# Kernel tuning notes

Measured on AMD Instinct MI355X. Metric: run time of the kernel, lower is better.

Reference implementation:

```python
import jax, jax.numpy as jnp
import numpy as np

N_DRUG, N_TARGET, N_EDGES, H = 50000, 20000, 500000, 256


def setup_inputs() -> dict:
    key = jax.random.key(0)
    ks = jax.random.split(key, 6)
    s = 1.0 / np.sqrt(2 * H)
    return {
        "z_drug": jax.random.normal(ks[0], (N_DRUG, H), dtype=jnp.float32),
        "z_target": jax.random.normal(ks[1], (N_TARGET, H), dtype=jnp.float32),
        "row": jax.random.randint(ks[2], (N_EDGES,), 0, N_DRUG, dtype=jnp.int64),
        "col": jax.random.randint(ks[3], (N_EDGES,), 0, N_TARGET, dtype=jnp.int64),
        "W1": jax.random.normal(ks[4], (2 * H, H), dtype=jnp.float32) * s,
        "b1": jnp.zeros((H,), dtype=jnp.float32),
        "W2": jax.random.normal(ks[5], (H, 1), dtype=jnp.float32) * (1.0 / np.sqrt(H)),
        "b2": jnp.zeros((1,), dtype=jnp.float32),
    }


def reference(z_drug, z_target, row, col, W1, b1, W2, b2):
    # gather endpoint embeddings by edge index, concat -> [E, 2H]
    zc = jnp.concatenate([z_drug[row], z_target[col]], axis=-1)
    h = jax.nn.relu(zc @ W1 + b1)          # [E, H]
    return h @ W2 + b2                     # [E, 1]
```

## Files before the change

### kernel.cpp

```cpp
#include <hip/hip_runtime.h>
#include <hip/hip_bf16.h>
#include <stdint.h>


typedef unsigned short u16;
typedef __attribute__((ext_vector_type(8))) short short8;
typedef __attribute__((ext_vector_type(4))) float f32x4;

#define HDIM 256
#define KDIM 512
#define BM 128
#define BK 64

__device__ __forceinline__ u16 f2bf(float f) {
  union { float f; uint32_t u; } v; v.f = f;
  uint32_t u = v.u;
  return (u16)((u + 0x7fffu + ((u >> 16) & 1u)) >> 16);
}

__device__ __forceinline__ void gl2lds16(const void* g, void* l) {
  __builtin_amdgcn_global_load_lds(
      (const __attribute__((address_space(1))) unsigned int*)g,
      (__attribute__((address_space(3))) unsigned int*)l,
      16, 0, 0);
}

__global__ void prep_kernel(const float* __restrict__ w1,
                            u16* __restrict__ w1t) {
  const int b = blockIdx.x;
  __shared__ float tile[64][65];
  const int k0 = (b >> 2) * 64, n0 = (b & 3) * 64;
  const int tx = threadIdx.x & 63, ty = threadIdx.x >> 6;
#pragma unroll
  for (int i = ty; i < 64; i += 4)
    tile[i][tx] = w1[(size_t)(k0 + i) * HDIM + n0 + tx];
  __syncthreads();
#pragma unroll
  for (int i = ty; i < 64; i += 4)
    w1t[(size_t)(n0 + i) * KDIM + k0 + tx] = f2bf(tile[tx][i]);
}

__global__ __launch_bounds__(256, 2) void edge_mlp_kernel(
    const float* __restrict__ zdf, const float* __restrict__ ztf,
    const int* __restrict__ row, const int* __restrict__ col,
    const u16* __restrict__ w1t, const float* __restrict__ b1,
    const float* __restrict__ w2, const float* __restrict__ b2,
    float* __restrict__ out, int E) {
  __shared__ u16 lB[2][HDIM * BK];

  const int tid   = threadIdx.x;
  const int wid   = tid >> 6;
  const int lane  = tid & 63;
  const int e0    = blockIdx.x * BM;
  const int r8    = lane >> 3;
  const int slog  = ((lane & 7) ^ (r8 & 7)) * 8;
  const int colid = lane & 15;
  const int quad  = lane >> 4;
  const int csw   = colid & 7;

  const u16* pB = w1t + (uint32_t)(wid * 64 + r8) * KDIM + slog;

  uint32_t offD2[2], offT2[2];
#pragma unroll
  for (int rt = 0; rt < 2; ++rt) {
    int ge = min(e0 + wid * 32 + rt * 16 + colid, E - 1);
    offD2[rt] = (uint32_t)row[ge] * HDIM;
    offT2[rt] = (uint32_t)col[ge] * HDIM;
  }

  f32x4 acc[2][16];
#pragma unroll
  for (int i = 0; i < 2; ++i)
#pragma unroll
    for (int j = 0; j < 16; ++j) acc[i][j] = f32x4{0.f, 0.f, 0.f, 0.f};

  float4 a32[2][2][2];
  short8 aB[2][2];

  auto loadA = [&](int kn) {
    const float* zb = (kn < 4) ? zdf : ztf;
    const uint32_t* offs = (kn < 4) ? offD2 : offT2;
    const int koffn = (kn & 3) * BK;
#pragma unroll
    for (int rt = 0; rt < 2; ++rt)
#pragma unroll
      for (int s = 0; s < 2; ++s) {
        const float* p = zb + offs[rt] + koffn + s * 32 + quad * 8;
        a32[rt][s][0] = ((const float4*)p)[0];
        a32[rt][s][1] = ((const float4*)p)[1];
      }
  };
  auto cvtA = [&]() {
#pragma unroll
    for (int rt = 0; rt < 2; ++rt)
#pragma unroll
      for (int s = 0; s < 2; ++s) {
        float4 lo = a32[rt][s][0], hi = a32[rt][s][1];
        short8 r;
        r[0] = (short)f2bf(lo.x); r[1] = (short)f2bf(lo.y);
        r[2] = (short)f2bf(lo.z); r[3] = (short)f2bf(lo.w);
        r[4] = (short)f2bf(hi.x); r[5] = (short)f2bf(hi.y);
        r[6] = (short)f2bf(hi.z); r[7] = (short)f2bf(hi.w);
        aB[rt][s] = r;
      }
  };

#pragma unroll
  for (int j = 0; j < 8; ++j)
    gl2lds16(pB + (size_t)j * 8 * KDIM, &lB[0][(wid * 64 + j * 8) * BK]);
  loadA(0);
  asm volatile("s_waitcnt vmcnt(0)" ::: "memory");
  cvtA();
  __builtin_amdgcn_s_barrier();

#pragma unroll
  for (int kc = 0; kc < 8; ++kc) {
    const int cur = kc & 1, nxt = cur ^ 1;
    if (kc < 7) {
      const int kn = kc + 1;
#pragma unroll
      for (int j = 0; j < 8; ++j)
        gl2lds16(pB + (size_t)j * 8 * KDIM + kn * BK,
                 &lB[nxt][(wid * 64 + j * 8) * BK]);
      loadA(kn);
    }
#pragma unroll
    for (int s = 0; s < 2; ++s) {
      const int sl = s * 4 + quad;
      __builtin_amdgcn_s_setprio(1);
#pragma unroll
      for (int ct = 0; ct < 16; ++ct) {
        short8 bF = *(const short8*)
            &lB[cur][(ct * 16 + colid) * BK + ((sl ^ csw) * 8)];
        acc[0][ct] = __builtin_amdgcn_mfma_f32_16x16x32_bf16(
            aB[0][s], bF, acc[0][ct], 0, 0, 0);
        acc[1][ct] = __builtin_amdgcn_mfma_f32_16x16x32_bf16(
            aB[1][s], bF, acc[1][ct], 0, 0, 0);
      }
      __builtin_amdgcn_s_setprio(0);
    }
    if (kc < 7) {
      asm volatile("s_waitcnt vmcnt(0)" ::: "memory");
      cvtA();
      __builtin_amdgcn_s_barrier();
    }
  }

  float b1v[16], w2v[16];
#pragma unroll
  for (int ct = 0; ct < 16; ++ct) {
    b1v[ct] = b1[ct * 16 + colid];
    w2v[ct] = w2[ct * 16 + colid];
  }
  const float b2v = b2[0];
#pragma unroll
  for (int rt = 0; rt < 2; ++rt)
#pragma unroll
    for (int j = 0; j < 4; ++j) {
      float s = 0.f;
#pragma unroll
      for (int ct = 0; ct < 16; ++ct)
        s += fmaxf(acc[rt][ct][j] + b1v[ct], 0.f) * w2v[ct];
#pragma unroll
      for (int off = 8; off >= 1; off >>= 1)
        s += __shfl_xor(s, off, 16);
      if (colid == 0) {
        int ge = e0 + wid * 32 + rt * 16 + quad * 4 + j;
        if (ge < E) out[ge] = s + b2v;
      }
    }
}

__global__ void fallback_kernel(
    const float* __restrict__ zd, const float* __restrict__ zt,
    const int* __restrict__ row, const int* __restrict__ col,
    const float* __restrict__ W1, const float* __restrict__ b1,
    const float* __restrict__ W2, const float* __restrict__ b2,
    float* __restrict__ out, int E) {
  __shared__ float zc[16][512];
  __shared__ float red[4][16];
  const int e0 = blockIdx.x * 16;
  const int tid = threadIdx.x;
  for (int i = tid; i < 16 * 512; i += 256) {
    int e = i >> 9, k = i & 511;
    int ge = min(e0 + e, E - 1);
    zc[e][k] = (k < HDIM) ? zd[(size_t)row[ge] * HDIM + k]
                          : zt[(size_t)col[ge] * HDIM + (k - HDIM)];
  }
  __syncthreads();
  float acc[16];
#pragma unroll
  for (int e = 0; e < 16; ++e) acc[e] = 0.f;
  for (int k = 0; k < KDIM; ++k) {
    float w = W1[k * HDIM + tid];
#pragma unroll
    for (int e = 0; e < 16; ++e) acc[e] += zc[e][k] * w;
  }
  float wv = W2[tid], bv = b1[tid];
  const int lane = tid & 63, wid = tid >> 6;
#pragma unroll
  for (int e = 0; e < 16; ++e) {
    float pv = fmaxf(acc[e] + bv, 0.f) * wv;
#pragma unroll
    for (int off = 32; off >= 1; off >>= 1) pv += __shfl_down(pv, off, 64);
    if (lane == 0) red[wid][e] = pv;
  }
  __syncthreads();
  if (tid < 16) {
    int ge = e0 + tid;
    if (ge < E)
      out[ge] = red[0][tid] + red[1][tid] + red[2][tid] + red[3][tid] + b2[0];
  }
}

extern "C" void kernel_launch(void* const* d_in, const int* in_sizes, int n_in,
                              void* d_out, int out_size, void* d_ws, size_t ws_size,
                              hipStream_t stream) {
  const float* zd_f = (const float*)d_in[0];
  const float* zt_f = (const float*)d_in[1];
  const int*   row  = (const int*)d_in[2];
  const int*   col  = (const int*)d_in[3];
  const float* W1   = (const float*)d_in[4];
  const float* b1   = (const float*)d_in[5];
  const float* W2   = (const float*)d_in[6];
  const float* b2   = (const float*)d_in[7];
  float* out = (float*)d_out;

  const int E = in_sizes[2];

  size_t need = (size_t)KDIM * HDIM * sizeof(u16);

  if (ws_size >= need) {
    u16* w1t = (u16*)d_ws;
    prep_kernel<<<32, 256, 0, stream>>>(W1, w1t);
    edge_mlp_kernel<<<(E + BM - 1) / BM, 256, 0, stream>>>(
        zd_f, zt_f, row, col, w1t, b1, W2, b2, out, E);
  } else {
    fallback_kernel<<<(E + 15) / 16, 256, 0, stream>>>(
        zd_f, zt_f, row, col, W1, b1, W2, b2, out, E);
  }
}
```

Before: 313.4 us.

## Factor first layer into per-node projections, gather fp16 results per edge

Splits W1 into drug and target halves and computes U = z_drug·W1_top and V = z_target·W1_bot once per node with an MFMA GEMM, stored as fp16. A separate edge kernel gathers U[row] and V[col], adds the bias, applies ReLU and takes the dot product with W2. This removes the per-edge 512×256 GEMM, replacing it with a much smaller node GEMM plus a bandwidth-bound gather. The cost is extra workspace, an extra kernel launch, and fp16 rounding of the intermediates.

After: 258.7 us. 1.21x faster.

```diff
diff --git a/kernel.cpp b/kernel.cpp
--- a/kernel.cpp
+++ b/kernel.cpp
@@ -9,13 +9,20 @@
 
 #define HDIM 256
 #define KDIM 512
-#define BM 128
 #define BK 64
 
 __device__ __forceinline__ u16 f2bf(float f) {
   union { float f; uint32_t u; } v; v.f = f;
   uint32_t u = v.u;
   return (u16)((u + 0x7fffu + ((u >> 16) & 1u)) >> 16);
+}
+__device__ __forceinline__ u16 f2h(float f) {
+  union { _Float16 h; u16 u; } v; v.h = (_Float16)f;
+  return v.u;
+}
+__device__ __forceinline__ float h2f(u16 b) {
+  union { _Float16 h; u16 u; } v; v.u = b;
+  return (float)v.h;
 }
 
 __device__ __forceinline__ void gl2lds16(const void* g, void* l) {
@@ -25,8 +32,7 @@
       16, 0, 0);
 }
 
-__global__ void prep_kernel(const float* __restrict__ w1,
-                            u16* __restrict__ w1t) {
+__global__ void prep_w1t(const float* __restrict__ w1, u16* __restrict__ w1t) {
   const int b = blockIdx.x;
   __shared__ float tile[64][65];
   const int k0 = (b >> 2) * 64, n0 = (b & 3) * 64;
@@ -40,135 +46,169 @@
     w1t[(size_t)(n0 + i) * KDIM + k0 + tx] = f2bf(tile[tx][i]);
 }
 
-__global__ __launch_bounds__(256, 2) void edge_mlp_kernel(
+__global__ __launch_bounds__(256, 2) void uv_gemm(
     const float* __restrict__ zdf, const float* __restrict__ ztf,
-    const int* __restrict__ row, const int* __restrict__ col,
-    const u16* __restrict__ w1t, const float* __restrict__ b1,
-    const float* __restrict__ w2, const float* __restrict__ b2,
-    float* __restrict__ out, int E) {
-  __shared__ u16 lB[2][HDIM * BK];
+    const u16* __restrict__ w1t, u16* __restrict__ Uh, u16* __restrict__ Vh,
+    int ND, int NT, int nUb) {
+  __shared__ u16 lB[2][128 * BK];
+
+  const int bid = blockIdx.x;
+  const int isV = (bid >= nUb);
+  const int lb  = isV ? (bid - nUb) : bid;
+  const float* zf = isV ? ztf : zdf;
+  u16* Oh = isV ? Vh : Uh;
+  const int NR = isV ? NT : ND;
+  const int r0 = (lb >> 1) * 128;
+  const int n0 = (lb & 1) * 128;
+  const int kb = isV ? 4 : 0;
 
   const int tid   = threadIdx.x;
   const int wid   = tid >> 6;
   const int lane  = tid & 63;
-  const int e0    = blockIdx.x * BM;
   const int r8    = lane >> 3;
   const int slog  = ((lane & 7) ^ (r8 & 7)) * 8;
   const int colid = lane & 15;
   const int quad  = lane >> 4;
   const int csw   = colid & 7;
 
-  const u16* pB = w1t + (uint32_t)(wid * 64 + r8) * KDIM + slog;
-
-  uint32_t offD2[2], offT2[2];
+  const u16* pB = w1t + (uint32_t)(n0 + wid * 32 + r8) * KDIM + slog;
+  u16* lBw0 = &lB[0][(wid * 32) * BK];
+  u16* lBw1 = &lB[1][(wid * 32) * BK];
+
+  uint32_t offR[2];
 #pragma unroll
   for (int rt = 0; rt < 2; ++rt) {
-    int ge = min(e0 + wid * 32 + rt * 16 + colid, E - 1);
-    offD2[rt] = (uint32_t)row[ge] * HDIM;
-    offT2[rt] = (uint32_t)col[ge] * HDIM;
-  }
-
-  f32x4 acc[2][16];
+    int r = min(r0 + wid * 32 + rt * 16 + colid, NR - 1);
+    offR[rt] = (uint32_t)r * HDIM;
+  }
+
+  f32x4 acc[2][8];
 #pragma unroll
   for (int i = 0; i < 2; ++i)
 #pragma unroll
-    for (int j = 0; j < 16; ++j) acc[i][j] = f32x4{0.f, 0.f, 0.f, 0.f};
-
-  float4 a32[2][2][2];
-  short8 aB[2][2];
-
-  auto loadA = [&](int kn) {
-    const float* zb = (kn < 4) ? zdf : ztf;
-    const uint32_t* offs = (kn < 4) ? offD2 : offT2;
-    const int koffn = (kn & 3) * BK;
+    for (int j = 0; j < 8; ++j) acc[i][j] = f32x4{0.f, 0.f, 0.f, 0.f};
+
+  float4 a32[2][2][2][2];
+  short8 aB[2][2][2];
+
+  auto loadA = [&](int kc, int buf) {
 #pragma unroll
     for (int rt = 0; rt < 2; ++rt)
 #pragma unroll
       for (int s = 0; s < 2; ++s) {
-        const float* p = zb + offs[rt] + koffn + s * 32 + quad * 8;
-        a32[rt][s][0] = ((const float4*)p)[0];
-        a32[rt][s][1] = ((const float4*)p)[1];
+        const float* p = zf + offR[rt] + kc * BK + s * 32 + quad * 8;
+        a32[buf][rt][s][0] = ((const float4*)p)[0];
+        a32[buf][rt][s][1] = ((const float4*)p)[1];
       }
   };
-  auto cvtA = [&]() {
+  auto cvtA = [&](int buf) {
 #pragma unroll
     for (int rt = 0; rt < 2; ++rt)
 #pragma unroll
       for (int s = 0; s < 2; ++s) {
-        float4 lo = a32[rt][s][0], hi = a32[rt][s][1];
+        float4 lo = a32[buf][rt][s][0], hi = a32[buf][rt][s][1];
         short8 r;
         r[0] = (short)f2bf(lo.x); r[1] = (short)f2bf(lo.y);
         r[2] = (short)f2bf(lo.z); r[3] = (short)f2bf(lo.w);
         r[4] = (short)f2bf(hi.x); r[5] = (short)f2bf(hi.y);
         r[6] = (short)f2bf(hi.z); r[7] = (short)f2bf(hi.w);
-        aB[rt][s] = r;
+        aB[buf][rt][s] = r;
       }
   };
-
-#pragma unroll
-  for (int j = 0; j < 8; ++j)
-    gl2lds16(pB + (size_t)j * 8 * KDIM, &lB[0][(wid * 64 + j * 8) * BK]);
-  loadA(0);
+  auto stageB = [&](int kch, u16* dst) {
+#pragma unroll
+    for (int t = 0; t < 4; ++t)
+      gl2lds16(pB + (size_t)t * 8 * KDIM + kch * BK, dst + t * 8 * BK);
+  };
+
+  stageB(kb, lBw0);
+  loadA(0, 0);
   asm volatile("s_waitcnt vmcnt(0)" ::: "memory");
-  cvtA();
+  cvtA(0);
   __builtin_amdgcn_s_barrier();
 
 #pragma unroll
-  for (int kc = 0; kc < 8; ++kc) {
+  for (int kc = 0; kc < 4; ++kc) {
     const int cur = kc & 1, nxt = cur ^ 1;
-    if (kc < 7) {
-      const int kn = kc + 1;
-#pragma unroll
-      for (int j = 0; j < 8; ++j)
-        gl2lds16(pB + (size_t)j * 8 * KDIM + kn * BK,
-                 &lB[nxt][(wid * 64 + j * 8) * BK]);
-      loadA(kn);
+    if (kc < 3) {
+      stageB(kb + kc + 1, nxt ? lBw1 : lBw0);
+      loadA(kc + 1, nxt);
     }
 #pragma unroll
     for (int s = 0; s < 2; ++s) {
       const int sl = s * 4 + quad;
       __builtin_amdgcn_s_setprio(1);
 #pragma unroll
-      for (int ct = 0; ct < 16; ++ct) {
+      for (int ct = 0; ct < 8; ++ct) {
         short8 bF = *(const short8*)
             &lB[cur][(ct * 16 + colid) * BK + ((sl ^ csw) * 8)];
         acc[0][ct] = __builtin_amdgcn_mfma_f32_16x16x32_bf16(
-            aB[0][s], bF, acc[0][ct], 0, 0, 0);
+            aB[cur][0][s], bF, acc[0][ct], 0, 0, 0);
         acc[1][ct] = __builtin_amdgcn_mfma_f32_16x16x32_bf16(
-            aB[1][s], bF, acc[1][ct], 0, 0, 0);
+            aB[cur][1][s], bF, acc[1][ct], 0, 0, 0);
       }
       __builtin_amdgcn_s_setprio(0);
     }
-    if (kc < 7) {
+    if (kc < 3) {
       asm volatile("s_waitcnt vmcnt(0)" ::: "memory");
-      cvtA();
+      cvtA(nxt);
       __builtin_amdgcn_s_barrier();
     }
   }
 
-  float b1v[16], w2v[16];
-#pragma unroll
-  for (int ct = 0; ct < 16; ++ct) {
-    b1v[ct] = b1[ct * 16 + colid];
-    w2v[ct] = w2[ct * 16 + colid];
+#pragma unroll
+  for (int rt = 0; rt < 2; ++rt)
+#pragma unroll
+    for (int j = 0; j < 4; ++j) {
+      int r = r0 + wid * 32 + rt * 16 + quad * 4 + j;
+      if (r < NR) {
+#pragma unroll
+        for (int ct = 0; ct < 8; ++ct)
+          Oh[(size_t)r * HDIM + n0 + ct * 16 + colid] = f2h(acc[rt][ct][j]);
+      }
+    }
+}
+
+__global__ __launch_bounds__(256, 4) void edge_kernel(
+    const u16* __restrict__ U, const u16* __restrict__ V,
+    const int* __restrict__ row, const int* __restrict__ col,
+    const float* __restrict__ b1, const float* __restrict__ w2,
+    const float* __restrict__ b2, float* __restrict__ out, int E) {
+  const int tid  = threadIdx.x;
+  const int lane = tid & 63;
+  const int wid  = tid >> 6;
+  const int li   = lane & 7;
+  const int eg   = lane >> 3;
+
+  float b1v[32], w2v[32];
+#pragma unroll
+  for (int i = 0; i < 32; ++i) {
+    b1v[i] = b1[li * 32 + i];
+    w2v[i] = w2[li * 32 + i];
   }
   const float b2v = b2[0];
-#pragma unroll
-  for (int rt = 0; rt < 2; ++rt)
-#pragma unroll
-    for (int j = 0; j < 4; ++j) {
-      float s = 0.f;
-#pragma unroll
-      for (int ct = 0; ct < 16; ++ct)
-        s += fmaxf(acc[rt][ct][j] + b1v[ct], 0.f) * w2v[ct];
-#pragma unroll
-      for (int off = 8; off >= 1; off >>= 1)
-        s += __shfl_xor(s, off, 16);
-      if (colid == 0) {
-        int ge = e0 + wid * 32 + rt * 16 + quad * 4 + j;
-        if (ge < E) out[ge] = s + b2v;
-      }
-    }
+
+  for (int base = blockIdx.x * 32; base < E; base += gridDim.x * 32) {
+    const int e  = base + wid * 8 + eg;
+    const int ee = min(e, E - 1);
+    const short8* up = (const short8*)(U + (size_t)row[ee] * HDIM + li * 32);
+    const short8* vp = (const short8*)(V + (size_t)col[ee] * HDIM + li * 32);
+    short8 ub[4], vb[4];
+#pragma unroll
+    for (int t = 0; t < 4; ++t) { ub[t] = up[t]; vb[t] = vp[t]; }
+    float s = 0.f;
+#pragma unroll
+    for (int t = 0; t < 4; ++t)
+#pragma unroll
+      for (int i = 0; i < 8; ++i) {
+        float h = h2f((u16)ub[t][i]) + h2f((u16)vb[t][i]) + b1v[t * 8 + i];
+        s += fmaxf(h, 0.f) * w2v[t * 8 + i];
+      }
+    s += __shfl_xor(s, 1, 8);
+    s += __shfl_xor(s, 2, 8);
+    s += __shfl_xor(s, 4, 8);
+    if (li == 0 && e < E) out[e] = s + b2v;
+  }
 }
 
 __global__ void fallback_kernel(
@@ -226,15 +266,28 @@
   const float* b2   = (const float*)d_in[7];
   float* out = (float*)d_out;
 
-  const int E = in_sizes[2];
-
-  size_t need = (size_t)KDIM * HDIM * sizeof(u16);
+  const int E  = in_sizes[2];
+  const int ND = in_sizes[0] / HDIM;
+  const int NT = in_sizes[1] / HDIM;
+
+  size_t off_w1t = 0;
+  size_t off_U   = (size_t)KDIM * HDIM * sizeof(u16);
+  size_t off_V   = off_U + (size_t)ND * HDIM * sizeof(u16);
+  size_t need    = off_V + (size_t)NT * HDIM * sizeof(u16);
 
   if (ws_size >= need) {
-    u16* w1t = (u16*)d_ws;
-    prep_kernel<<<32, 256, 0, stream>>>(W1, w1t);
-    edge_mlp_kernel<<<(E + BM - 1) / BM, 256, 0, stream>>>(
-        zd_f, zt_f, row, col, w1t, b1, W2, b2, out, E);
+    u16* w1t = (u16*)((char*)d_ws + off_w1t);
+    u16* Uh  = (u16*)((char*)d_ws + off_U);
+    u16* Vh  = (u16*)((char*)d_ws + off_V);
+    const int nUb = ((ND + 127) / 128) * 2;
+    const int nVb = ((NT + 127) / 128) * 2;
+    prep_w1t<<<32, 256, 0, stream>>>(W1, w1t);
+    uv_gemm<<<nUb + nVb, 256, 0, stream>>>(zd_f, zt_f, w1t, Uh, Vh,
+                                           ND, NT, nUb);
+    int egrid = (E + 31) / 32;
+    if (egrid > 2048) egrid = 2048;
+    edge_kernel<<<egrid, 256, 0, stream>>>(Uh, Vh, row, col, b1, W2, b2,
+                                           out, E);
   } else {
     fallback_kernel<<<(E + 15) / 16, 256, 0, stream>>>(
         zd_f, zt_f, row, col, W1, b1, W2, b2, out, E);
```
